# Kernel tuning notes

Measured on AMD Instinct MI355X. Metric: run time of the kernel, lower is better.

The kernel has to match this reference:

```python
import jax, jax.numpy as jnp
import numpy as np

D_MODEL = 1024
N_HEADS = 16
D_K = D_MODEL // N_HEADS  # 64, also d_v
B, S = 8, 1024


def setup_inputs() -> dict:
    key = jax.random.key(0)
    ks = jax.random.split(key, 12)
    sc = 1.0 / np.sqrt(D_MODEL)
    inp = {
        "q": jax.random.normal(ks[0], (B, S, D_MODEL), jnp.float32),
        "k": jax.random.normal(ks[1], (B, S, D_MODEL), jnp.float32),
        "v": jax.random.normal(ks[2], (B, S, D_MODEL), jnp.float32),
        # per-head projection weights stacked over heads; torch Linear stores [out,in]
        "Wq": jax.random.normal(ks[3], (N_HEADS, D_K, D_MODEL), jnp.float32) * sc,
        "bq": jax.random.normal(ks[4], (N_HEADS, D_K), jnp.float32) * sc,
        "Wk": jax.random.normal(ks[5], (N_HEADS, D_K, D_MODEL), jnp.float32) * sc,
        "bk": jax.random.normal(ks[6], (N_HEADS, D_K), jnp.float32) * sc,
        "Wv": jax.random.normal(ks[7], (N_HEADS, D_K, D_MODEL), jnp.float32) * sc,
        "bv": jax.random.normal(ks[8], (N_HEADS, D_K), jnp.float32) * sc,
        "Wf": jax.random.normal(ks[9], (D_MODEL, D_MODEL), jnp.float32) * sc,
        "bf": jax.random.normal(ks[10], (D_MODEL,), jnp.float32) * sc,
    }
    return inp


def reference(q, k, v, Wq, bq, Wk, bk, Wv, bv, Wf, bf):
    temper = jnp.asarray(D_K ** 0.5, q.dtype)
    # per-head linear projections, all heads at once: [b,s,h,dk]
    qh = jnp.einsum('bsd,hkd->bhsk', q, Wq) + bq[None, :, None, :]
    kh = jnp.einsum('bsd,hkd->bhsk', k, Wk) + bk[None, :, None, :]
    vh = jnp.einsum('bsd,hkd->bhsk', v, Wv) + bv[None, :, None, :]
    # scaled dot-product scores [b,h,s,s]
    scores = jnp.einsum('bhik,bhjk->bhij', qh, kh) / temper
    # faithful scalar-equality mask: positions exactly equal to mask (=0) -> -inf
    scores = jnp.where(scores == 0.0, -jnp.inf, scores)
    attn = jax.nn.softmax(scores, axis=-1)
    out = jnp.einsum('bhij,bhjv->bhiv', attn, vh)  # [b,h,s,dv]
    # concat heads (head order matches torch.cat over ModuleList)
    out = out.transpose(0, 2, 1, 3).reshape(out.shape[0], out.shape[2], -1)  # [b,s,d_model]
    return out @ Wf.T + bf
```

## Files before the change

### kernel.cpp

```cpp
#include <hip/hip_runtime.h>
#include <hip/hip_bf16.h>


#define D_MODEL_ 1024
#define NH_ 16
#define DK_ 64
#define B_ 8
#define S_ 1024
#define M_ (B_ * S_)

typedef __hip_bfloat16 bf16;
typedef __attribute__((ext_vector_type(8))) short short8;
typedef __attribute__((ext_vector_type(4))) short short4_t;
typedef __attribute__((ext_vector_type(4))) float f32x4;

typedef const __attribute__((address_space(1))) unsigned int* gas_u32p;
typedef __attribute__((address_space(3))) unsigned int* las_u32p;

__device__ __forceinline__ short f2bs(float x) {
  bf16 h = __float2bfloat16(x);
  return *reinterpret_cast<short*>(&h);
}

__global__ __launch_bounds__(256)
void conv_w4(const float* __restrict__ w0, const float* __restrict__ w1,
             const float* __restrict__ w2, const float* __restrict__ w3,
             bf16* __restrict__ out) {
  const float* src = (blockIdx.z == 0) ? w0 : (blockIdx.z == 1) ? w1
                   : (blockIdx.z == 2) ? w2 : w3;
  size_t i = ((size_t)blockIdx.x * 256 + threadIdx.x) * 8;
  f32x4 a = *(const f32x4*)(src + i);
  f32x4 b = *(const f32x4*)(src + i + 4);
  short8 s;
  s[0] = f2bs(a[0]); s[1] = f2bs(a[1]); s[2] = f2bs(a[2]); s[3] = f2bs(a[3]);
  s[4] = f2bs(b[0]); s[5] = f2bs(b[1]); s[6] = f2bs(b[2]); s[7] = f2bs(b[3]);
  *(short8*)((short*)out + (size_t)blockIdx.z * 1024 * 1024 + i) = s;
}

template<int BN, int AF32>
__device__ __forceinline__ void gemm_body(const void* __restrict__ A,
                                          const bf16* __restrict__ Wb,
                                          const float* __restrict__ bias,
                                          void* __restrict__ C,
                                          int cMode, float cscale, int m0, int n0)
{
  __shared__ short As[2][128 * 32];
  __shared__ short Bs[2][BN * 32];
  const int tid = threadIdx.x;
  const int lane = tid & 63;
  const int w = tid >> 6;
  const int l15 = lane & 15, quad = lane >> 4;
  const int wm = (w >> 1) * 64, wn = (w & 1) * (BN / 2);
  const int srow = lane >> 2;
  const int sslot = ((lane & 3) ^ ((lane >> 3) & 3)) * 8;
  const int rsl = (quad ^ ((l15 >> 1) & 3)) * 8;

  f32x4 au[4], av[4];
  auto loadAf = [&](int k0) {
    const float* Af = (const float*)A;
#pragma unroll
    for (int p = 0; p < 4; ++p) {
      int c = p * 256 + tid;
      int r = c >> 3, kc = (c & 7) * 8;
      const float* g = Af + (size_t)(m0 + r) * 1024 + k0 + kc;
      au[p] = *(const f32x4*)g;
      av[p] = *(const f32x4*)(g + 4);
    }
  };
  auto writeAf = [&]() {
#pragma unroll
    for (int p = 0; p < 4; ++p) {
      int c = p * 256 + tid;
      int r = c >> 3, kc = (c & 7) * 8;
      int s = (c & 3) ^ ((r >> 1) & 3);
      short8 sv;
      sv[0] = f2bs(au[p][0]); sv[1] = f2bs(au[p][1]); sv[2] = f2bs(au[p][2]); sv[3] = f2bs(au[p][3]);
      sv[4] = f2bs(av[p][0]); sv[5] = f2bs(av[p][1]); sv[6] = f2bs(av[p][2]); sv[7] = f2bs(av[p][3]);
      *(short8*)&As[kc >> 5][r * 32 + s * 8] = sv;
    }
  };

  f32x4 acc[4][BN / 32];
#pragma unroll
  for (int i = 0; i < 4; ++i)
#pragma unroll
    for (int j = 0; j < BN / 32; ++j)
      acc[i][j] = (f32x4){0.f, 0.f, 0.f, 0.f};

  if (AF32) loadAf(0);

  for (int k0 = 0; k0 < 1024; k0 += 64) {
    __syncthreads();
    if (AF32) {
      writeAf();
    } else {
      const bf16* Ab = (const bf16*)A;
#pragma unroll
      for (int sub = 0; sub < 2; ++sub)
#pragma unroll
        for (int p = 0; p < 2; ++p) {
          int r = 32 * w + 16 * p + srow;
          __builtin_amdgcn_global_load_lds(
              (gas_u32p)(const void*)(Ab + (size_t)(m0 + r) * 1024 + k0 + sub * 32 + sslot),
              (las_u32p)(void*)((char*)&As[sub][0] + w * 2048 + p * 1024), 16, 0, 0);
        }
    }
#pragma unroll
    for (int sub = 0; sub < 2; ++sub)
#pragma unroll
      for (int p = 0; p < BN / 64; ++p) {
        int r = (BN / 4) * w + 16 * p + srow;
        __builtin_amdgcn_global_load_lds(
            (gas_u32p)(const void*)(Wb + (size_t)(n0 + r) * 1024 + k0 + sub * 32 + sslot),
            (las_u32p)(void*)((char*)&Bs[sub][0] + w * (BN / 4) * 64 + p * 1024), 16, 0, 0);
      }
    __syncthreads();

    if (AF32 && k0 + 64 < 1024) loadAf(k0 + 64);

#pragma unroll
    for (int kk = 0; kk < 2; ++kk) {
      short8 af[4], bfv[BN / 32];
#pragma unroll
      for (int t = 0; t < 4; ++t)
        af[t]  = *(short8*)&As[kk][(wm + t * 16 + l15) * 32 + rsl];
#pragma unroll
      for (int t = 0; t < BN / 32; ++t)
        bfv[t] = *(short8*)&Bs[kk][(wn + t * 16 + l15) * 32 + rsl];
#pragma unroll
      for (int mt = 0; mt < 4; ++mt)
#pragma unroll
        for (int nt = 0; nt < BN / 32; ++nt)
          acc[mt][nt] = __builtin_amdgcn_mfma_f32_16x16x32_bf16(af[mt], bfv[nt], acc[mt][nt], 0, 0, 0);
    }
  }

  if (cMode == 2) {
    bf16* vt = (bf16*)C;
    const int bidx = m0 >> 10;
    const int sbase = (m0 & 1023) + wm;
#pragma unroll
    for (int nt = 0; nt < BN / 32; ++nt) {
      int n = n0 + wn + nt * 16 + l15;
      float bv = bias[n];
#pragma unroll
      for (int mt = 0; mt < 4; ++mt) {
        int s = sbase + mt * 16 + quad * 4;
        short4_t pk;
#pragma unroll
        for (int r = 0; r < 4; ++r) pk[r] = f2bs((acc[mt][nt][r] + bv) * cscale);
        *(short4_t*)((short*)vt + ((size_t)bidx * 1024 + n) * 1024 + s) = pk;
      }
    }
  } else {
#pragma unroll
    for (int nt = 0; nt < BN / 32; ++nt) {
      int col = n0 + wn + nt * 16 + l15;
      float bv = bias[col];
#pragma unroll
      for (int mt = 0; mt < 4; ++mt)
#pragma unroll
        for (int r = 0; r < 4; ++r) {
          int row = m0 + wm + mt * 16 + quad * 4 + r;
          float val = (acc[mt][nt][r] + bv) * cscale;
          if (cMode == 1) ((float*)C)[(size_t)row * 1024 + col] = val;
          else ((bf16*)C)[(size_t)row * 1024 + col] = __float2bfloat16(val);
        }
    }
  }
}

__global__ __launch_bounds__(256)
void gemm_proj(const float* __restrict__ q, const float* __restrict__ k,
               const float* __restrict__ v, const bf16* __restrict__ wq,
               const bf16* __restrict__ wk, const bf16* __restrict__ wv,
               const float* __restrict__ bq, const float* __restrict__ bk,
               const float* __restrict__ bv, void* __restrict__ cq,
               void* __restrict__ ck, void* __restrict__ cv)
{
  const int z = blockIdx.z;
  const float* A = (z == 0) ? q : (z == 1) ? k : v;
  const bf16* W  = (z == 0) ? wq : (z == 1) ? wk : wv;
  const float* bb = (z == 0) ? bq : (z == 1) ? bk : bv;
  void* C = (z == 0) ? cq : (z == 1) ? ck : cv;
  int cMode = (z == 2) ? 2 : 0;
  float cscale = (z == 0) ? 0.125f : 1.0f;
  gemm_body<128, 1>(A, W, bb, C, cMode, cscale, blockIdx.x * 128, blockIdx.y * 128);
}

__global__ __launch_bounds__(256)
void gemm_final(const bf16* __restrict__ A, const bf16* __restrict__ W,
                const float* __restrict__ bias, void* __restrict__ C)
{
  gemm_body<64, 0>(A, W, bias, C, 1, 1.0f, blockIdx.x * 128, blockIdx.y * 64);
}

__global__ __launch_bounds__(256)
void attn_mfma(const bf16* __restrict__ QH, const bf16* __restrict__ KH,
               const bf16* __restrict__ VT, bf16* __restrict__ AO)
{
  __shared__ short Ks[2][64 * 32];
  __shared__ short Vs[2][64 * 32];
  __shared__ short Ps[4][16 * 72];
  const int tid = threadIdx.x;
  const int lane = tid & 63;
  const int w = tid >> 6;
  const int l15 = lane & 15, quad = lane >> 4;
  const int q0 = blockIdx.x * 64;
  const int h = blockIdx.y, b = blockIdx.z;
  const size_t base = ((size_t)b * S_) * D_MODEL_ + (size_t)h * DK_;
  const size_t vtb  = (((size_t)b * NH_ + h) * DK_) * (size_t)S_;
  const float NEG = -1e30f;
  short* myPs = Ps[w];

  const int srow = 16 * w + (lane >> 2);
  const int sslot = ((lane & 3) ^ ((lane >> 3) & 3)) * 8;
  const int rsl = (quad ^ ((l15 >> 1) & 3)) * 8;

  short8 qa[2];
#pragma unroll
  for (int ks = 0; ks < 2; ++ks)
    qa[ks] = *(const short8*)((const short*)QH + base + (size_t)(q0 + w * 16 + l15) * D_MODEL_ + ks * 32 + quad * 8);

  float mi = NEG, li = 0.f;
  f32x4 oacc[4];
#pragma unroll
  for (int nt = 0; nt < 4; ++nt) oacc[nt] = (f32x4){0.f, 0.f, 0.f, 0.f};

  for (int j0 = 0; j0 < S_; j0 += 64) {
    __syncthreads();
#pragma unroll
    for (int sub = 0; sub < 2; ++sub) {
      __builtin_amdgcn_global_load_lds(
          (gas_u32p)(const void*)((const short*)KH + base + (size_t)(j0 + srow) * D_MODEL_ + sub * 32 + sslot),
          (las_u32p)(void*)((char*)&Ks[sub][0] + w * 1024), 16, 0, 0);
      __builtin_amdgcn_global_load_lds(
          (gas_u32p)(const void*)((const short*)VT + vtb + (size_t)srow * S_ + j0 + sub * 32 + sslot),
          (las_u32p)(void*)((char*)&Vs[sub][0] + w * 1024), 16, 0, 0);
    }
    __syncthreads();

    short8 kb[4][2], vb[4][2];
#pragma unroll
    for (int nt = 0; nt < 4; ++nt)
#pragma unroll
      for (int ks = 0; ks < 2; ++ks) {
        kb[nt][ks] = *(short8*)&Ks[ks][(nt * 16 + l15) * 32 + rsl];
        vb[nt][ks] = *(short8*)&Vs[ks][(nt * 16 + l15) * 32 + rsl];
      }

    f32x4 sacc[4];
#pragma unroll
    for (int nt = 0; nt < 4; ++nt) sacc[nt] = (f32x4){0.f, 0.f, 0.f, 0.f};
    __builtin_amdgcn_s_setprio(1);
#pragma unroll
    for (int nt = 0; nt < 4; ++nt)
#pragma unroll
      for (int ks = 0; ks < 2; ++ks)
        sacc[nt] = __builtin_amdgcn_mfma_f32_16x16x32_bf16(kb[nt][ks], qa[ks], sacc[nt], 0, 0, 0);
    __builtin_amdgcn_s_setprio(0);

    float p[4][4];
#pragma unroll
    for (int nt = 0; nt < 4; ++nt)
#pragma unroll
      for (int r = 0; r < 4; ++r) {
        float x = sacc[nt][r];
        if (x == 0.0f) x = NEG;
        p[nt][r] = x;
      }
    float mm[4];
#pragma unroll
    for (int nt = 0; nt < 4; ++nt)
      mm[nt] = fmaxf(fmaxf(p[nt][0], p[nt][1]), fmaxf(p[nt][2], p[nt][3]));
    float rm = fmaxf(fmaxf(mm[0], mm[1]), fmaxf(mm[2], mm[3]));
    rm = fmaxf(rm, __shfl_xor(rm, 16, 64));
    rm = fmaxf(rm, __shfl_xor(rm, 32, 64));

    const bool skip = __all(rm <= mi + 8.0f);
    const float nm = skip ? mi : fmaxf(mi, rm);

    float psum[4];
#pragma unroll
    for (int nt = 0; nt < 4; ++nt) {
      float e0 = __expf(p[nt][0] - nm), e1 = __expf(p[nt][1] - nm);
      float e2 = __expf(p[nt][2] - nm), e3 = __expf(p[nt][3] - nm);
      p[nt][0] = e0; p[nt][1] = e1; p[nt][2] = e2; p[nt][3] = e3;
      psum[nt] = (e0 + e1) + (e2 + e3);
    }
    float ps = (psum[0] + psum[1]) + (psum[2] + psum[3]);
    ps += __shfl_xor(ps, 16, 64);
    ps += __shfl_xor(ps, 32, 64);

    if (skip) {
      li += ps;
    } else {
      float alpha = __expf(mi - nm);
      li = li * alpha + ps;
      float ar[4];
#pragma unroll
      for (int r = 0; r < 4; ++r) ar[r] = __shfl(alpha, quad * 4 + r, 64);
#pragma unroll
      for (int nt = 0; nt < 4; ++nt)
#pragma unroll
        for (int r = 0; r < 4; ++r) oacc[nt][r] *= ar[r];
    }
    mi = nm;

#pragma unroll
    for (int nt = 0; nt < 4; ++nt) {
      short4_t pk;
#pragma unroll
      for (int r = 0; r < 4; ++r) pk[r] = f2bs(p[nt][r]);
      *(short4_t*)&myPs[l15 * 72 + nt * 16 + quad * 4] = pk;
    }

    __threadfence_block();

    short8 pa[2];
#pragma unroll
    for (int ks = 0; ks < 2; ++ks)
      pa[ks] = *(short8*)&myPs[l15 * 72 + ks * 32 + quad * 8];
    __builtin_amdgcn_s_setprio(1);
#pragma unroll
    for (int nt = 0; nt < 4; ++nt)
#pragma unroll
      for (int ks = 0; ks < 2; ++ks)
        oacc[nt] = __builtin_amdgcn_mfma_f32_16x16x32_bf16(pa[ks], vb[nt][ks], oacc[nt], 0, 0, 0);
    __builtin_amdgcn_s_setprio(0);
  }

  float lr[4];
#pragma unroll
  for (int r = 0; r < 4; ++r) lr[r] = __shfl(li, quad * 4 + r, 64);
#pragma unroll
  for (int r = 0; r < 4; ++r) {
    float inv = (lr[r] > 0.f) ? 1.0f / lr[r] : 0.f;
    int q = q0 + w * 16 + quad * 4 + r;
#pragma unroll
    for (int nt = 0; nt < 4; ++nt)
      AO[base + (size_t)q * D_MODEL_ + nt * 16 + l15] = __float2bfloat16(oacc[nt][r] * inv);
  }
}

extern "C" void kernel_launch(void* const* d_in, const int* in_sizes, int n_in,
                              void* d_out, int out_size, void* d_ws, size_t ws_size,
                              hipStream_t stream) {
  (void)in_sizes; (void)n_in; (void)out_size;
  const float* q  = (const float*)d_in[0];
  const float* k  = (const float*)d_in[1];
  const float* v  = (const float*)d_in[2];
  const float* Wq = (const float*)d_in[3];
  const float* bq = (const float*)d_in[4];
  const float* Wk = (const float*)d_in[5];
  const float* bk = (const float*)d_in[6];
  const float* Wv = (const float*)d_in[7];
  const float* bv = (const float*)d_in[8];
  const float* Wf = (const float*)d_in[9];
  const float* bF = (const float*)d_in[10];

  const size_t MB = (size_t)1024 * 1024;
  char* ws = (char*)d_ws;
  bf16* wqb = (bf16*)(ws);
  bf16* wkb = (bf16*)(ws + 2 * MB);
  bf16* wvb = (bf16*)(ws + 4 * MB);
  bf16* wfb = (bf16*)(ws + 6 * MB);
  bf16* vt  = (bf16*)(ws + 8 * MB);
  bf16* qh  = (bf16*)d_out;
  bf16* kh  = (bf16*)((char*)d_out + 16 * MB);

  const bool bigws = ws_size >= (size_t)40 * MB;
  bf16* aob = bigws ? (bf16*)(ws + 24 * MB) : qh;
  bf16* fin = bigws ? aob : (bf16*)(ws + 8 * MB);

  dim3 blk(256);

  conv_w4<<<dim3(512, 1, 4), blk, 0, stream>>>(Wq, Wk, Wv, Wf, wqb);

  gemm_proj<<<dim3(M_ / 128, D_MODEL_ / 128, 3), blk, 0, stream>>>(
      q, k, v, wqb, wkb, wvb, bq, bk, bv, qh, kh, vt);

  attn_mfma<<<dim3(S_ / 64, NH_, B_), blk, 0, stream>>>(qh, kh, vt, aob);

  if (!bigws)
    hipMemcpyAsync(ws + 8 * MB, d_out, 16 * MB, hipMemcpyDeviceToDevice, stream);

  gemm_final<<<dim3(M_ / 128, D_MODEL_ / 64), blk, 0, stream>>>(fin, wfb, bF, d_out);
}
```

Before: 330.3 us.

## Register-prefetch GEMM tiles and fold log2e into Q scale for exp2 softmax

Replaces the direct global-to-LDS loads of the bf16 A and W tiles in the GEMM body with a register-staged prefetch. The next k-step's tiles are loaded into registers while the MFMA loop runs and written into swizzled LDS at the top of each iteration, using raw barriers and an explicit lgkmcnt wait. Separately, the Q projection scale now includes log2(e), so the attention softmax can use exp2f instead of __expf, and the lazy-rescale threshold is adjusted to match. The prefetch adds register pressure and relies on hand-placed waits and barriers being correct.

```diff
diff --git a/kernel.cpp b/kernel.cpp
--- a/kernel.cpp
+++ b/kernel.cpp
@@ -51,86 +51,105 @@
   const int w = tid >> 6;
   const int l15 = lane & 15, quad = lane >> 4;
   const int wm = (w >> 1) * 64, wn = (w & 1) * (BN / 2);
-  const int srow = lane >> 2;
-  const int sslot = ((lane & 3) ^ ((lane >> 3) & 3)) * 8;
   const int rsl = (quad ^ ((l15 >> 1) & 3)) * 8;
 
+  constexpr int NPB = BN / 32;
+
   f32x4 au[4], av[4];
-  auto loadAf = [&](int k0) {
-    const float* Af = (const float*)A;
-#pragma unroll
-    for (int p = 0; p < 4; ++p) {
-      int c = p * 256 + tid;
-      int r = c >> 3, kc = (c & 7) * 8;
-      const float* g = Af + (size_t)(m0 + r) * 1024 + k0 + kc;
-      au[p] = *(const f32x4*)g;
-      av[p] = *(const f32x4*)(g + 4);
+  short8 ab[4];
+  short8 bb[NPB];
+
+  auto loadA = [&](int k0) {
+    if (AF32) {
+      const float* Af = (const float*)A;
+#pragma unroll
+      for (int p = 0; p < 4; ++p) {
+        int c = p * 256 + tid;
+        int r = c >> 3, kc = (c & 7) * 8;
+        const float* g = Af + (size_t)(m0 + r) * 1024 + k0 + kc;
+        au[p] = *(const f32x4*)g;
+        av[p] = *(const f32x4*)(g + 4);
+      }
+    } else {
+      const bf16* Ab = (const bf16*)A;
+#pragma unroll
+      for (int p = 0; p < 4; ++p) {
+        int c = p * 256 + tid;
+        int r = c >> 3, kc = (c & 7) * 8;
+        ab[p] = *(const short8*)((const short*)Ab + (size_t)(m0 + r) * 1024 + k0 + kc);
+      }
     }
   };
-  auto writeAf = [&]() {
+  auto writeA = [&]() {
 #pragma unroll
     for (int p = 0; p < 4; ++p) {
       int c = p * 256 + tid;
       int r = c >> 3, kc = (c & 7) * 8;
       int s = (c & 3) ^ ((r >> 1) & 3);
-      short8 sv;
-      sv[0] = f2bs(au[p][0]); sv[1] = f2bs(au[p][1]); sv[2] = f2bs(au[p][2]); sv[3] = f2bs(au[p][3]);
-      sv[4] = f2bs(av[p][0]); sv[5] = f2bs(av[p][1]); sv[6] = f2bs(av[p][2]); sv[7] = f2bs(av[p][3]);
-      *(short8*)&As[kc >> 5][r * 32 + s * 8] = sv;
+      if (AF32) {
+        short8 sv;
+        sv[0] = f2bs(au[p][0]); sv[1] = f2bs(au[p][1]); sv[2] = f2bs(au[p][2]); sv[3] = f2bs(au[p][3]);
+        sv[4] = f2bs(av[p][0]); sv[5] = f2bs(av[p][1]); sv[6] = f2bs(av[p][2]); sv[7] = f2bs(av[p][3]);
+        *(short8*)&As[kc >> 5][r * 32 + s * 8] = sv;
+      } else {
+        *(short8*)&As[kc >> 5][r * 32 + s * 8] = ab[p];
+      }
     }
   };
-
-  f32x4 acc[4][BN / 32];
+  auto loadB = [&](int k0) {
+#pragma unroll
+    for (int p = 0; p < NPB; ++p) {
+      int c = p * 256 + tid;
+      int r = c >> 3, kc = (c & 7) * 8;
+      bb[p] = *(const short8*)((const short*)Wb + (size_t)(n0 + r) * 1024 + k0 + kc);
+    }
+  };
+  auto writeB = [&]() {
+#pragma unroll
+    for (int p = 0; p < NPB; ++p) {
+      int c = p * 256 + tid;
+      int r = c >> 3, kc = (c & 7) * 8;
+      int s = (c & 3) ^ ((r >> 1) & 3);
+      *(short8*)&Bs[kc >> 5][r * 32 + s * 8] = bb[p];
+    }
+  };
+
+  f32x4 acc[4][NPB];
 #pragma unroll
   for (int i = 0; i < 4; ++i)
 #pragma unroll
-    for (int j = 0; j < BN / 32; ++j)
+    for (int j = 0; j < NPB; ++j)
       acc[i][j] = (f32x4){0.f, 0.f, 0.f, 0.f};
 
-  if (AF32) loadAf(0);
+  loadA(0);
+  loadB(0);
 
   for (int k0 = 0; k0 < 1024; k0 += 64) {
-    __syncthreads();
-    if (AF32) {
-      writeAf();
-    } else {
-      const bf16* Ab = (const bf16*)A;
-#pragma unroll
-      for (int sub = 0; sub < 2; ++sub)
-#pragma unroll
-        for (int p = 0; p < 2; ++p) {
-          int r = 32 * w + 16 * p + srow;
-          __builtin_amdgcn_global_load_lds(
-              (gas_u32p)(const void*)(Ab + (size_t)(m0 + r) * 1024 + k0 + sub * 32 + sslot),
-              (las_u32p)(void*)((char*)&As[sub][0] + w * 2048 + p * 1024), 16, 0, 0);
-        }
-    }
-#pragma unroll
-    for (int sub = 0; sub < 2; ++sub)
-#pragma unroll
-      for (int p = 0; p < BN / 64; ++p) {
-        int r = (BN / 4) * w + 16 * p + srow;
-        __builtin_amdgcn_global_load_lds(
-            (gas_u32p)(const void*)(Wb + (size_t)(n0 + r) * 1024 + k0 + sub * 32 + sslot),
-            (las_u32p)(void*)((char*)&Bs[sub][0] + w * (BN / 4) * 64 + p * 1024), 16, 0, 0);
-      }
-    __syncthreads();
-
-    if (AF32 && k0 + 64 < 1024) loadAf(k0 + 64);
+    __builtin_amdgcn_s_barrier();
+    writeA();
+    writeB();
+    asm volatile("s_waitcnt lgkmcnt(0)" ::: "memory");
+    __builtin_amdgcn_s_barrier();
+    __builtin_amdgcn_sched_barrier(0);
+
+    if (k0 + 64 < 1024) {
+      loadA(k0 + 64);
+      loadB(k0 + 64);
+    }
 
 #pragma unroll
     for (int kk = 0; kk < 2; ++kk) {
-      short8 af[4], bfv[BN / 32];
+      short8 af[4], bfv[NPB];
 #pragma unroll
       for (int t = 0; t < 4; ++t)
         af[t]  = *(short8*)&As[kk][(wm + t * 16 + l15) * 32 + rsl];
 #pragma unroll
-      for (int t = 0; t < BN / 32; ++t)
+      for (int t = 0; t < NPB; ++t)
         bfv[t] = *(short8*)&Bs[kk][(wn + t * 16 + l15) * 32 + rsl];
 #pragma unroll
       for (int mt = 0; mt < 4; ++mt)
 #pragma unroll
-        for (int nt = 0; nt < BN / 32; ++nt)
+        for (int nt = 0; nt < NPB; ++nt)
           acc[mt][nt] = __builtin_amdgcn_mfma_f32_16x16x32_bf16(af[mt], bfv[nt], acc[mt][nt], 0, 0, 0);
     }
   }
@@ -140,7 +159,7 @@
     const int bidx = m0 >> 10;
     const int sbase = (m0 & 1023) + wm;
 #pragma unroll
-    for (int nt = 0; nt < BN / 32; ++nt) {
+    for (int nt = 0; nt < NPB; ++nt) {
       int n = n0 + wn + nt * 16 + l15;
       float bv = bias[n];
 #pragma unroll
@@ -154,7 +173,7 @@
     }
   } else {
 #pragma unroll
-    for (int nt = 0; nt < BN / 32; ++nt) {
+    for (int nt = 0; nt < NPB; ++nt) {
       int col = n0 + wn + nt * 16 + l15;
       float bv = bias[col];
 #pragma unroll
@@ -184,7 +203,7 @@
   const float* bb = (z == 0) ? bq : (z == 1) ? bk : bv;
   void* C = (z == 0) ? cq : (z == 1) ? ck : cv;
   int cMode = (z == 2) ? 2 : 0;
-  float cscale = (z == 0) ? 0.125f : 1.0f;
+  float cscale = (z == 0) ? 0.18033688011112042f : 1.0f;
   gemm_body<128, 1>(A, W, bb, C, cMode, cscale, blockIdx.x * 128, blockIdx.y * 128);
 }
 
@@ -211,6 +230,7 @@
   const size_t base = ((size_t)b * S_) * D_MODEL_ + (size_t)h * DK_;
   const size_t vtb  = (((size_t)b * NH_ + h) * DK_) * (size_t)S_;
   const float NEG = -1e30f;
+  const float THR = 11.54156032f;
   short* myPs = Ps[w];
 
   const int srow = 16 * w + (lane >> 2);
@@ -277,14 +297,14 @@
     rm = fmaxf(rm, __shfl_xor(rm, 16, 64));
     rm = fmaxf(rm, __shfl_xor(rm, 32, 64));
 
-    const bool skip = __all(rm <= mi + 8.0f);
+    const bool skip = __all(rm <= mi + THR);
     const float nm = skip ? mi : fmaxf(mi, rm);
 
     float psum[4];
 #pragma unroll
     for (int nt = 0; nt < 4; ++nt) {
-      float e0 = __expf(p[nt][0] - nm), e1 = __expf(p[nt][1] - nm);
-      float e2 = __expf(p[nt][2] - nm), e3 = __expf(p[nt][3] - nm);
+      float e0 = exp2f(p[nt][0] - nm), e1 = exp2f(p[nt][1] - nm);
+      float e2 = exp2f(p[nt][2] - nm), e3 = exp2f(p[nt][3] - nm);
       p[nt][0] = e0; p[nt][1] = e1; p[nt][2] = e2; p[nt][3] = e3;
       psum[nt] = (e0 + e1) + (e2 + e3);
     }
@@ -295,7 +315,7 @@
     if (skip) {
       li += ps;
     } else {
-      float alpha = __expf(mi - nm);
+      float alpha = exp2f(mi - nm);
       li = li * alpha + ps;
       float ar[4];
 #pragma unroll
```

After: 333.9 us. No clear change (+1.1%).
